# Performance work log

Measured on AMD Instinct MI355X. Metric: run time of the kernel, lower is better.

The kernel has to match this reference:

```python
import jax, jax.numpy as jnp
import numpy as np

PH = PW = 128   # patch size
SH = SW = 64    # stride
H = W = 512     # image size
NH = (H - (PH - SH)) // SH  # 7 patches vertically
NW = (W - (PW - SW)) // SW  # 7 patches horizontally
N, C = 8, 3


def _patch_weight(up, down, left, right):
    # Faithful vectorization of getPatchWeight (nested if/elif per pixel).
    Wl, Hl = PW - SW, PH - SH
    j = np.arange(PW)
    wd = np.where((j < PW - SW) & (not left), j,
         np.where((j > SW) & (not right), PW - j, Wl))
    i = np.arange(PH)
    hd = np.where((i < PH - SH) & (not up), i,
         np.where((i > SH) & (not down), PH - i, Hl))
    return (hd[:, None] * wd[None, :]).astype(np.float32) / float(Wl * Hl)


def _weight_map():
    # [NH, NW, PH, PW] weight per grid position, exact elif order of forward()
    ctr = _patch_weight(0, 0, 0, 0)
    UL = _patch_weight(1, 0, 1, 0); UR = _patch_weight(1, 0, 0, 1)
    DL = _patch_weight(0, 1, 1, 0); DR = _patch_weight(0, 1, 0, 1)
    U = _patch_weight(1, 0, 0, 0); Dw = _patch_weight(0, 1, 0, 0)
    L = _patch_weight(0, 0, 1, 0); R = _patch_weight(0, 0, 0, 1)
    wmap = np.zeros((NH, NW, PH, PW), np.float32)
    for i in range(NH):
        for j in range(NW):
            if i == 0 and j == 0: w = UL
            elif i == 0 and j == NW - 1: w = UR
            elif i == NH - 1 and j == 0: w = DL
            elif i == NH - 1 and j == NW - 1: w = DR
            elif i == 0: w = U
            elif j == 0: w = L
            elif i == NW - 1: w = Dw  # replicates original's numW-based check
            elif j == NW - 1: w = R
            else: w = ctr
            wmap[i, j] = w
    return jnp.asarray(wmap)

_WMAP = _weight_map()


def setup_inputs() -> dict:
    key = jax.random.key(0)
    ks = jax.random.split(key, 8)
    return {
        "inputTensor": jax.random.normal(ks[0], (N, C, H, W), jnp.float32),
        "inputNorm":   jax.random.normal(ks[1], (N, 3, H, W), jnp.float32),
        "W_albedo":  jax.random.normal(ks[2], (3, 6), jnp.float32) * 0.1,
        "b_albedo":  jnp.zeros((3,), jnp.float32),
        "W_normal":  jax.random.normal(ks[3], (3, 6), jnp.float32) * 0.1,
        "b_normal":  jnp.zeros((3,), jnp.float32),
        "W_shading": jax.random.normal(ks[4], (3, 6), jnp.float32) * 0.1,
        "b_shading": jnp.zeros((3,), jnp.float32),
        "W_light":   jax.random.normal(ks[5], (27, 6), jnp.float32) * 0.1,
        "b_light":   jnp.zeros((27,), jnp.float32),
    }


def reference(inputTensor, inputNorm, W_albedo, b_albedo, W_normal, b_normal,
              W_shading, b_shading, W_light, b_light):
    # ---- patch extraction (vectorized unfold) ----
    idx_h = jnp.arange(NH)[:, None] * SH + jnp.arange(PH)[None, :]   # [NH, PH]
    idx_w = jnp.arange(NW)[:, None] * SW + jnp.arange(PW)[None, :]   # [NW, PW]
    # [N, C, NH, NW, PH, PW]
    in_p = inputTensor[:, :, idx_h[:, None, :, None], idx_w[None, :, None, :]]
    nm_p = inputNorm[:, :, idx_h[:, None, :, None], idx_w[None, :, None, :]]
    feat = jnp.concatenate([in_p, nm_p], axis=1)  # [N, 6, NH, NW, PH, PW]

    # ---- stand-in subNetwork: per-pixel 1x1 heads + pooled lighting head ----
    def head(Wm, b):
        return jnp.tanh(jnp.einsum('oc,nchwpq->nohwpq', Wm, feat)
                        + b[None, :, None, None, None, None])

    albedo_p = head(W_albedo, b_albedo)    # [N,3,NH,NW,PH,PW]
    normal_p = head(W_normal, b_normal)
    shading_p = head(W_shading, b_shading)
    pooled = feat.mean(axis=(4, 5))                              # [N,6,NH,NW]
    lighting = jnp.einsum('oc,nchw->nohw', W_light, pooled) \
        + b_light[None, :, None, None]                           # [N,27,NH,NW]

    # ---- weighted overlap-add stitching (vectorized fold) ----
    def stitch(p):
        wp = p * _WMAP[None, None]
        out = jnp.zeros((p.shape[0], 3, H, W), p.dtype)
        return out.at[:, :, idx_h[:, None, :, None],
                      idx_w[None, :, None, :]].add(wp)

    out_albedo = stitch(albedo_p)
    out_normal = stitch(normal_p)
    out_shading = stitch(shading_p)

    # ---- overlap consistency loss on shading (L1 mean per pair, summed) ----
    Wl, Hl = PW - SW, PH - SH
    h_diff = shading_p[:, :, :, 1:, :, :Wl] - shading_p[:, :, :, :-1, :, SW:]
    v_diff = shading_p[:, :, 1:, :, :Hl, :] - shading_p[:, :, :-1, :, SH:, :]
    loss_h = jnp.sum(jnp.abs(h_diff)) / (N * 3 * PH * Wl)
    loss_v = jnp.sum(jnp.abs(v_diff)) / (N * 3 * Hl * PW)
    overlap_loss = (loss_h + loss_v) / (NH * NW)

    return out_albedo, out_normal, out_shading, lighting, overlap_loss
```

## Files before the change

### kernel.cpp

```cpp
#include <hip/hip_runtime.h>

#define NBATCH 8
#define HH 512
#define WW 512
#define NPIX (HH * WW)
#define IMG_ELEMS (NBATCH * 3 * NPIX)
#define OFF_ALBEDO 0
#define OFF_NORMAL ((size_t)IMG_ELEMS)
#define OFF_SHADING ((size_t)(2 * IMG_ELEMS))
#define OFF_LIGHT ((size_t)(3 * IMG_ELEMS))
#define N_LIGHT (NBATCH * 27 * 49)
#define OFF_LOSS (OFF_LIGHT + N_LIGHT)
#define NBLK (NBATCH * 8 * 8 * 4)

__device__ __forceinline__ float fast_tanh(float x) {
    float e = __expf(2.0f * x);
    return 1.0f - 2.0f / (e + 1.0f);
}

__global__ __launch_bounds__(256) void fused_heads_kernel(
    const float* __restrict__ inT, const float* __restrict__ inN,
    const float* __restrict__ Wa, const float* __restrict__ ba,
    const float* __restrict__ Wn, const float* __restrict__ bn,
    const float* __restrict__ Ws, const float* __restrict__ bs,
    float* __restrict__ out, float* __restrict__ P) {
    int bid = blockIdx.x;
    int n = bid >> 8;
    int rem = bid & 255;
    int ti = rem >> 5;
    int rem2 = rem & 31;
    int tj = rem2 >> 2;
    int rc = rem2 & 3;

    int t = threadIdx.x;
    int rowc = t >> 4;
    int col4 = t & 15;
    int y = ti * 64 + rc * 16 + rowc;
    int x = tj * 64 + col4 * 4;

    float4 f[6];
    size_t base = ((size_t)(n * 3) * HH + y) * WW + x;
#pragma unroll
    for (int c = 0; c < 3; ++c) {
        f[c]     = *reinterpret_cast<const float4*>(inT + base + (size_t)c * NPIX);
        f[c + 3] = *reinterpret_cast<const float4*>(inN + base + (size_t)c * NPIX);
    }

    size_t obase = ((size_t)(n * 3) * HH + y) * WW + x;
#pragma unroll
    for (int h = 0; h < 3; ++h) {
        const float* W = (h == 0) ? Wa : (h == 1) ? Wn : Ws;
        const float* b = (h == 0) ? ba : (h == 1) ? bn : bs;
        float* o_ptr = out + ((h == 0) ? OFF_ALBEDO : (h == 1) ? OFF_NORMAL : OFF_SHADING);
#pragma unroll
        for (int o = 0; o < 3; ++o) {
            float bv = b[o];
            float ax = bv, ay = bv, az = bv, aw = bv;
#pragma unroll
            for (int c = 0; c < 6; ++c) {
                float w = W[o * 6 + c];
                ax = fmaf(w, f[c].x, ax);
                ay = fmaf(w, f[c].y, ay);
                az = fmaf(w, f[c].z, az);
                aw = fmaf(w, f[c].w, aw);
            }
            float4 r;
            r.x = fast_tanh(ax);
            r.y = fast_tanh(ay);
            r.z = fast_tanh(az);
            r.w = fast_tanh(aw);
            *reinterpret_cast<float4*>(o_ptr + obase + (size_t)o * NPIX) = r;
        }
    }

    float s[6];
#pragma unroll
    for (int c = 0; c < 6; ++c) s[c] = f[c].x + f[c].y + f[c].z + f[c].w;

#pragma unroll
    for (int off = 32; off > 0; off >>= 1) {
#pragma unroll
        for (int c = 0; c < 6; ++c) s[c] += __shfl_down(s[c], off, 64);
    }

    __shared__ float red[4][6];
    int wave = t >> 6;
    int lane = t & 63;
    if (lane == 0) {
#pragma unroll
        for (int c = 0; c < 6; ++c) red[wave][c] = s[c];
    }
    __syncthreads();
    if (t < 6) {
        float v = red[0][t] + red[1][t] + red[2][t] + red[3][t];
        P[(size_t)bid * 8 + t] = v;
    }
}

__global__ __launch_bounds__(256) void lighting_kernel(
    const float* __restrict__ P, const float* __restrict__ Wl,
    const float* __restrict__ bl, float* __restrict__ out) {
    int tid = blockIdx.x * blockDim.x + threadIdx.x;
    if (tid > N_LIGHT) return;
    if (tid == N_LIGHT) {
        out[OFF_LOSS] = 0.0f;
        return;
    }
    int n = tid / (27 * 49);
    int r = tid % (27 * 49);
    int o = r / 49;
    int r2 = r % 49;
    int i = r2 / 7;
    int j = r2 % 7;

    float s[6] = {0.f, 0.f, 0.f, 0.f, 0.f, 0.f};
#pragma unroll
    for (int di = 0; di < 2; ++di) {
#pragma unroll
        for (int dj = 0; dj < 2; ++dj) {
            int ti = i + di;
            int tj = j + dj;
            int bbase = ((n * 8 + ti) * 8 + tj) * 4;
#pragma unroll
            for (int rc = 0; rc < 4; ++rc) {
                const float* p = P + (size_t)(bbase + rc) * 8;
#pragma unroll
                for (int c = 0; c < 6; ++c) s[c] += p[c];
            }
        }
    }
    float acc = bl[o];
#pragma unroll
    for (int c = 0; c < 6; ++c)
        acc = fmaf(Wl[o * 6 + c], s[c] * (1.0f / 16384.0f), acc);
    out[OFF_LIGHT + tid] = acc;
}

extern "C" void kernel_launch(void* const* d_in, const int* in_sizes, int n_in,
                              void* d_out, int out_size, void* d_ws, size_t ws_size,
                              hipStream_t stream) {
    const float* inT = (const float*)d_in[0];
    const float* inN = (const float*)d_in[1];
    const float* Wa = (const float*)d_in[2];
    const float* ba = (const float*)d_in[3];
    const float* Wn = (const float*)d_in[4];
    const float* bn = (const float*)d_in[5];
    const float* Ws = (const float*)d_in[6];
    const float* bs = (const float*)d_in[7];
    const float* Wl = (const float*)d_in[8];
    const float* bl = (const float*)d_in[9];
    float* out = (float*)d_out;
    float* P = (float*)d_ws;

    fused_heads_kernel<<<NBLK, 256, 0, stream>>>(
        inT, inN, Wa, ba, Wn, bn, Ws, bs, out, P);

    lighting_kernel<<<(N_LIGHT + 1 + 255) / 256, 256, 0, stream>>>(P, Wl, bl, out);
}
```

Measured before the change: 30.11 us.

## Double per-thread work and use nontemporal loads/stores in fused heads kernel

```diff
diff --git a/kernel.cpp b/kernel.cpp
--- a/kernel.cpp
+++ b/kernel.cpp
@@ -11,11 +11,20 @@
 #define OFF_LIGHT ((size_t)(3 * IMG_ELEMS))
 #define N_LIGHT (NBATCH * 27 * 49)
 #define OFF_LOSS (OFF_LIGHT + N_LIGHT)
-#define NBLK (NBATCH * 8 * 8 * 4)
+#define NBLK (NBATCH * 8 * 8 * 2)
+
+typedef float f32x4 __attribute__((ext_vector_type(4)));
 
 __device__ __forceinline__ float fast_tanh(float x) {
     float e = __expf(2.0f * x);
     return 1.0f - 2.0f / (e + 1.0f);
+}
+
+__device__ __forceinline__ f32x4 nt_load4(const float* p) {
+    return __builtin_nontemporal_load(reinterpret_cast<const f32x4*>(p));
+}
+__device__ __forceinline__ void nt_store4(float* p, f32x4 v) {
+    __builtin_nontemporal_store(v, reinterpret_cast<f32x4*>(p));
 }
 
 __global__ __launch_bounds__(256) void fused_heads_kernel(
@@ -25,25 +34,27 @@
     const float* __restrict__ Ws, const float* __restrict__ bs,
     float* __restrict__ out, float* __restrict__ P) {
     int bid = blockIdx.x;
-    int n = bid >> 8;
-    int rem = bid & 255;
-    int ti = rem >> 5;
-    int rem2 = rem & 31;
-    int tj = rem2 >> 2;
-    int rc = rem2 & 3;
+    int n = bid >> 7;
+    int rem = bid & 127;
+    int ti = rem >> 4;
+    int rem2 = rem & 15;
+    int tj = rem2 >> 1;
+    int half = rem2 & 1;
 
     int t = threadIdx.x;
-    int rowc = t >> 4;
-    int col4 = t & 15;
-    int y = ti * 64 + rc * 16 + rowc;
-    int x = tj * 64 + col4 * 4;
+    int rowc = t >> 3;
+    int col8 = t & 7;
+    int y = ti * 64 + half * 32 + rowc;
+    int x = tj * 64 + col8 * 8;
 
-    float4 f[6];
+    f32x4 fa[6], fb[6];
     size_t base = ((size_t)(n * 3) * HH + y) * WW + x;
 #pragma unroll
     for (int c = 0; c < 3; ++c) {
-        f[c]     = *reinterpret_cast<const float4*>(inT + base + (size_t)c * NPIX);
-        f[c + 3] = *reinterpret_cast<const float4*>(inN + base + (size_t)c * NPIX);
+        fa[c]     = nt_load4(inT + base + (size_t)c * NPIX);
+        fb[c]     = nt_load4(inT + base + (size_t)c * NPIX + 4);
+        fa[c + 3] = nt_load4(inN + base + (size_t)c * NPIX);
+        fb[c + 3] = nt_load4(inN + base + (size_t)c * NPIX + 4);
     }
 
     size_t obase = ((size_t)(n * 3) * HH + y) * WW + x;
@@ -55,27 +66,32 @@
 #pragma unroll
         for (int o = 0; o < 3; ++o) {
             float bv = b[o];
-            float ax = bv, ay = bv, az = bv, aw = bv;
+            f32x4 A = {bv, bv, bv, bv};
+            f32x4 B = {bv, bv, bv, bv};
 #pragma unroll
             for (int c = 0; c < 6; ++c) {
                 float w = W[o * 6 + c];
-                ax = fmaf(w, f[c].x, ax);
-                ay = fmaf(w, f[c].y, ay);
-                az = fmaf(w, f[c].z, az);
-                aw = fmaf(w, f[c].w, aw);
+                A.x = fmaf(w, fa[c].x, A.x);
+                A.y = fmaf(w, fa[c].y, A.y);
+                A.z = fmaf(w, fa[c].z, A.z);
+                A.w = fmaf(w, fa[c].w, A.w);
+                B.x = fmaf(w, fb[c].x, B.x);
+                B.y = fmaf(w, fb[c].y, B.y);
+                B.z = fmaf(w, fb[c].z, B.z);
+                B.w = fmaf(w, fb[c].w, B.w);
             }
-            float4 r;
-            r.x = fast_tanh(ax);
-            r.y = fast_tanh(ay);
-            r.z = fast_tanh(az);
-            r.w = fast_tanh(aw);
-            *reinterpret_cast<float4*>(o_ptr + obase + (size_t)o * NPIX) = r;
+            f32x4 rA = {fast_tanh(A.x), fast_tanh(A.y), fast_tanh(A.z), fast_tanh(A.w)};
+            f32x4 rB = {fast_tanh(B.x), fast_tanh(B.y), fast_tanh(B.z), fast_tanh(B.w)};
+            nt_store4(o_ptr + obase + (size_t)o * NPIX, rA);
+            nt_store4(o_ptr + obase + (size_t)o * NPIX + 4, rB);
         }
     }
 
     float s[6];
 #pragma unroll
-    for (int c = 0; c < 6; ++c) s[c] = f[c].x + f[c].y + f[c].z + f[c].w;
+    for (int c = 0; c < 6; ++c)
+        s[c] = (fa[c].x + fa[c].y + fa[c].z + fa[c].w) +
+               (fb[c].x + fb[c].y + fb[c].z + fb[c].w);
 
 #pragma unroll
     for (int off = 32; off > 0; off >>= 1) {
@@ -120,10 +136,10 @@
         for (int dj = 0; dj < 2; ++dj) {
             int ti = i + di;
             int tj = j + dj;
-            int bbase = ((n * 8 + ti) * 8 + tj) * 4;
 #pragma unroll
-            for (int rc = 0; rc < 4; ++rc) {
-                const float* p = P + (size_t)(bbase + rc) * 8;
+            for (int half = 0; half < 2; ++half) {
+                int b = ((n * 8 + ti) * 8 + tj) * 2 + half;
+                const float* p = P + (size_t)b * 8;
 #pragma unroll
                 for (int c = 0; c < 6; ++c) s[c] += p[c];
             }
```

Result: slower. 56.01 us (+86.0%).
